# Performance work log

Measured on AMD Instinct MI355X. Metric: run time of the kernel, lower is better.

## Reference

```python
import jax, jax.numpy as jnp
import numpy as np

S, N, H = 4096, 32, 512

def setup_inputs() -> dict:
    key = jax.random.key(0)
    ks = jax.random.split(key, 8)
    scale = 1.0 / np.sqrt(H)
    return {
        "hidden": jax.random.normal(ks[0], (N, H), dtype=jnp.float32),
        "encoder_outputs": jax.random.normal(ks[1], (S, N, H), dtype=jnp.float32),
        "W_w": jax.random.uniform(ks[2], (H, H), jnp.float32, -scale, scale),
        "W_b": jax.random.uniform(ks[3], (H,), jnp.float32, -scale, scale),
        "U_w": jax.random.uniform(ks[4], (H, H), jnp.float32, -scale, scale),
        "U_b": jax.random.uniform(ks[5], (H,), jnp.float32, -scale, scale),
        "v_w": jax.random.uniform(ks[6], (1, H), jnp.float32, -scale, scale),
        "v_b": jax.random.uniform(ks[7], (1,), jnp.float32, -scale, scale),
    }

def reference(hidden, encoder_outputs, W_w, W_b, U_w, U_b, v_w, v_b):
    # W(hidden): [N,H] -> broadcast over seq dim (equivalent to expand then Linear)
    wh = hidden @ W_w.T + W_b                      # [N, H]
    ue = jnp.einsum('snh,kh->snk', encoder_outputs, U_w) + U_b  # [S, N, H]
    energy = jnp.tanh(wh[None, :, :] + ue)         # [S, N, H]
    score = jnp.einsum('snh,oh->sno', energy, v_w) + v_b        # [S, N, 1]
    attention_weights = jax.nn.softmax(score, axis=0)           # softmax over seq
    context = jnp.sum(attention_weights * encoder_outputs, axis=0)  # [N, H]
    return (context, attention_weights)
```

## Files before the change

kernel.cpp:

```cpp
#include <hip/hip_runtime.h>
#include <hip/hip_bf16.h>

#define Sdim 4096
#define Ndim 32
#define Hdim 512
#define Mdim (Sdim * Ndim)

#define BM 128
#define BN 256
#define BK 32

typedef __bf16 bf16x8 __attribute__((ext_vector_type(8)));
typedef float f32x4 __attribute__((ext_vector_type(4)));
typedef unsigned short ushort8v __attribute__((ext_vector_type(8)));

__device__ __forceinline__ void load_lds16(const void* g, void* l) {
    __builtin_amdgcn_global_load_lds(
        (const __attribute__((address_space(1))) void*)g,
        (__attribute__((address_space(3))) void*)l, 16, 0, 0);
}

__device__ __forceinline__ float ftanh(float x) {
    float e = __expf(2.f * x);
    return 1.f - 2.f / (e + 1.f);
}

__global__ __launch_bounds__(256) void k_prep_bias(
    const float* __restrict__ hidden, const float* __restrict__ Ww,
    const float* __restrict__ Wb, const float* __restrict__ Ubias,
    float* __restrict__ bias) {
    const int t = threadIdx.x, w = t >> 6, lane = t & 63;
    const int cc = blockIdx.x * 4 + w;
    const float4 w0 = *(const float4*)(Ww + (size_t)cc * Hdim + lane * 8);
    const float4 w1 = *(const float4*)(Ww + (size_t)cc * Hdim + lane * 8 + 4);
    const float wb = Wb[cc] + Ubias[cc];
    for (int n = 0; n < Ndim; ++n) {
        const float4 h0 = *(const float4*)(hidden + n * Hdim + lane * 8);
        const float4 h1 = *(const float4*)(hidden + n * Hdim + lane * 8 + 4);
        float p = w0.x * h0.x + w0.y * h0.y + w0.z * h0.z + w0.w * h0.w +
                  w1.x * h1.x + w1.y * h1.y + w1.z * h1.z + w1.w * h1.w;
        p += __shfl_xor(p, 1);  p += __shfl_xor(p, 2);
        p += __shfl_xor(p, 4);  p += __shfl_xor(p, 8);
        p += __shfl_xor(p, 16); p += __shfl_xor(p, 32);
        if (lane == 0) bias[n * Hdim + cc] = p + wb;
    }
}

__global__ __launch_bounds__(256) void k_cvt(
    const float* __restrict__ src, unsigned short* __restrict__ dst) {
    const int i = blockIdx.x * 256 + threadIdx.x;
    float4 v = ((const float4*)src)[i];
    union { __hip_bfloat162 h[2]; ushort4 u; } r;
    r.h[0] = __float22bfloat162_rn(make_float2(v.x, v.y));
    r.h[1] = __float22bfloat162_rn(make_float2(v.z, v.w));
    ((ushort4*)dst)[i] = r.u;
}

__global__ __launch_bounds__(512, 4) void k_gemm_score(
    const float* __restrict__ enc,
    const unsigned short* __restrict__ Ub,
    const float* __restrict__ bias,
    const float* __restrict__ vw,
    float* __restrict__ scorep) {
    __shared__ __align__(16) unsigned short Asm[BM][40];
    __shared__ __align__(16) unsigned short Bsm[BN * BK];
    __shared__ float ssm[4][BM];

    const int t = threadIdx.x;
    const int lane = t & 63;
    const int w = t >> 6;
    const int wM = w >> 2;
    const int wN = w & 3;
    const int c = lane & 15;
    const int q = lane >> 4;

    const int rowblk = blockIdx.x >> 1;
    const int colblk = blockIdx.x & 1;
    const int mBase = rowblk * BM;
    const int colBase = colblk * BN;

    const int ar = t >> 2;
    const int aq = t & 3;
    const int asw = ((ar >> 3) & 1) << 1;
    const float* aptr = enc + (size_t)(mBase + ar) * Hdim + aq * 8;
    unsigned short* awr = &Asm[ar][(aq ^ asw) * 8];

    const int bsw = (lane & 3) ^ ((lane >> 4) & 3);
    const unsigned short* bptr0 =
        Ub + (size_t)(colBase + w * 16 + (lane >> 2)) * Hdim + bsw * 8;
    const unsigned short* bptr1 =
        Ub + (size_t)(colBase + 128 + w * 16 + (lane >> 2)) * Hdim + bsw * 8;
    unsigned short* bdst0 = &Bsm[(w * 16) * BK];
    unsigned short* bdst1 = &Bsm[(128 + w * 16) * BK];

    const int sA = ((c >> 3) & 1) << 1;
    const int sB = c >> 2;

    f32x4 acc[4][4];
#pragma unroll
    for (int i = 0; i < 4; ++i)
#pragma unroll
        for (int j = 0; j < 4; ++j) acc[i][j] = (f32x4){0.f, 0.f, 0.f, 0.f};

    for (int kk = 0; kk < Hdim / BK; ++kk) {
        __syncthreads();
        const float4 f0 = *(const float4*)(aptr + kk * BK);
        const float4 f1 = *(const float4*)(aptr + kk * BK + 4);
        union { __hip_bfloat162 h[4]; ushort8v v; } pk;
        pk.h[0] = __float22bfloat162_rn(make_float2(f0.x, f0.y));
        pk.h[1] = __float22bfloat162_rn(make_float2(f0.z, f0.w));
        pk.h[2] = __float22bfloat162_rn(make_float2(f1.x, f1.y));
        pk.h[3] = __float22bfloat162_rn(make_float2(f1.z, f1.w));
        *(ushort8v*)awr = pk.v;
        load_lds16(bptr0 + kk * BK, bdst0);
        load_lds16(bptr1 + kk * BK, bdst1);
        __syncthreads();

        bf16x8 af[4], bfr[4];
#pragma unroll
        for (int mi = 0; mi < 4; ++mi)
            af[mi] = *(const bf16x8*)&Asm[wM * 64 + mi * 16 + c][(q ^ sA) * 8];
#pragma unroll
        for (int ni = 0; ni < 4; ++ni) {
            const int col = wN * 64 + ni * 16 + c;
            bfr[ni] = *(const bf16x8*)&Bsm[col * BK + (q ^ sB) * 8];
        }
#pragma unroll
        for (int mi = 0; mi < 4; ++mi)
#pragma unroll
            for (int ni = 0; ni < 4; ++ni)
                acc[mi][ni] = __builtin_amdgcn_mfma_f32_16x16x32_bf16(
                    af[mi], bfr[ni], acc[mi][ni], 0, 0, 0);
    }

    float vcol[4];
#pragma unroll
    for (int ni = 0; ni < 4; ++ni) vcol[ni] = vw[colBase + wN * 64 + ni * 16 + c];

#pragma unroll
    for (int mi = 0; mi < 4; ++mi) {
#pragma unroll
        for (int reg = 0; reg < 4; ++reg) {
            const int rl = wM * 64 + mi * 16 + q * 4 + reg;
            const int n = rl & 31;
            float p = 0.f;
#pragma unroll
            for (int ni = 0; ni < 4; ++ni) {
                const int col = colBase + wN * 64 + ni * 16 + c;
                float e = acc[mi][ni][reg] + bias[n * Hdim + col];
                p += vcol[ni] * ftanh(e);
            }
            p += __shfl_xor(p, 1);
            p += __shfl_xor(p, 2);
            p += __shfl_xor(p, 4);
            p += __shfl_xor(p, 8);
            if (c == 0) ssm[wN][rl] = p;
        }
    }
    __syncthreads();
    if (t < BM) {
        const int m = mBase + t;
        const float s = ssm[0][t] + ssm[1][t] + ssm[2][t] + ssm[3][t];
        scorep[colblk * Mdim + (m & 31) * Sdim + (m >> 5)] = s;
    }
}

__global__ __launch_bounds__(256) void k_softmax(
    const float* __restrict__ scorep,
    float* __restrict__ out_w) {
    const int n = blockIdx.x;
    const int t = threadIdx.x;
    const int w = t >> 6;
    __shared__ float row[Sdim];
    __shared__ float red[8];
    const float4* s0 = (const float4*)(scorep + n * Sdim);
    const float4* s1 = (const float4*)(scorep + Mdim + n * Sdim);

    float mx = -1e30f;
    for (int i = t; i < Sdim / 4; i += 256) {
        float4 a = s0[i], b = s1[i];
        float4 v;
        v.x = a.x + b.x; v.y = a.y + b.y; v.z = a.z + b.z; v.w = a.w + b.w;
        ((float4*)row)[i] = v;
        mx = fmaxf(mx, fmaxf(fmaxf(v.x, v.y), fmaxf(v.z, v.w)));
    }
#pragma unroll
    for (int o = 32; o > 0; o >>= 1) mx = fmaxf(mx, __shfl_xor(mx, o));
    if ((t & 63) == 0) red[w] = mx;
    __syncthreads();
    mx = fmaxf(fmaxf(red[0], red[1]), fmaxf(red[2], red[3]));

    float sum = 0.f;
    for (int i = t; i < Sdim; i += 256) sum += __expf(row[i] - mx);
#pragma unroll
    for (int o = 32; o > 0; o >>= 1) sum += __shfl_xor(sum, o);
    if ((t & 63) == 0) red[4 + w] = sum;
    __syncthreads();
    sum = red[4] + red[5] + red[6] + red[7];
    const float inv = 1.f / sum;
    for (int i = t; i < Sdim; i += 256)
        out_w[i * Ndim + n] = __expf(row[i] - mx) * inv;
}

__global__ __launch_bounds__(256) void k_context(
    const float* __restrict__ enc, const float* __restrict__ wts,
    float* __restrict__ part) {
    const int n = blockIdx.x & 31;
    const int sc = blockIdx.x >> 5;
    const int s0 = sc * 256;
    const int t = threadIdx.x;
    const int hv = t & 127;
    const int sl = t >> 7;
    float4 a0 = {0.f, 0.f, 0.f, 0.f}, a1 = {0.f, 0.f, 0.f, 0.f};
    for (int i = sl * 2; i < 256; i += 4) {
        const float w0 = wts[(size_t)(s0 + i) * Ndim + n];
        const float w1 = wts[(size_t)(s0 + i + 1) * Ndim + n];
        const float4 e0 =
            *(const float4*)(enc + ((size_t)(s0 + i) * Ndim + n) * Hdim + hv * 4);
        const float4 e1 =
            *(const float4*)(enc + ((size_t)(s0 + i + 1) * Ndim + n) * Hdim + hv * 4);
        a0.x += w0 * e0.x; a0.y += w0 * e0.y; a0.z += w0 * e0.z; a0.w += w0 * e0.w;
        a1.x += w1 * e1.x; a1.y += w1 * e1.y; a1.z += w1 * e1.z; a1.w += w1 * e1.w;
    }
    a0.x += a1.x; a0.y += a1.y; a0.z += a1.z; a0.w += a1.w;
    __shared__ float4 red[128];
    if (sl == 1) red[hv] = a0;
    __syncthreads();
    if (sl == 0) {
        const float4 b = red[hv];
        float4 r;
        r.x = a0.x + b.x; r.y = a0.y + b.y; r.z = a0.z + b.z; r.w = a0.w + b.w;
        *(float4*)(part + (size_t)(sc * 32 + n) * Hdim + hv * 4) = r;
    }
}

__global__ __launch_bounds__(256) void k_ctx_reduce(
    const float* __restrict__ part, float* __restrict__ out) {
    const int j = blockIdx.x * 256 + threadIdx.x;
    float4 s = {0.f, 0.f, 0.f, 0.f};
    for (int i = 0; i < 16; ++i) {
        const float4 v = ((const float4*)part)[i * 4096 + j];
        s.x += v.x; s.y += v.y; s.z += v.z; s.w += v.w;
    }
    ((float4*)out)[j] = s;
}

extern "C" void kernel_launch(void* const* d_in, const int* in_sizes, int n_in,
                              void* d_out, int out_size, void* d_ws,
                              size_t ws_size, hipStream_t stream) {
    const float* hidden = (const float*)d_in[0];
    const float* enc    = (const float*)d_in[1];
    const float* Ww     = (const float*)d_in[2];
    const float* Wb     = (const float*)d_in[3];
    const float* Uw     = (const float*)d_in[4];
    const float* Ubias  = (const float*)d_in[5];
    const float* vw     = (const float*)d_in[6];

    float* out = (float*)d_out;

    char* ws = (char*)d_ws;
    float* bias          = (float*)(ws);
    unsigned short* Ub16 = (unsigned short*)(ws + (64 << 10));
    float* scorep        = (float*)(ws + (576 << 10));
    float* part          = (float*)(ws + (64 << 10));

    k_prep_bias<<<128, 256, 0, stream>>>(hidden, Ww, Wb, Ubias, bias);
    k_cvt<<<256, 256, 0, stream>>>(Uw, Ub16);
    k_gemm_score<<<(Mdim / BM) * 2, 512, 0, stream>>>(enc, Ub16, bias, vw,
                                                      scorep);
    k_softmax<<<Ndim, 256, 0, stream>>>(scorep, out + Ndim * Hdim);
    k_context<<<Ndim * (Sdim / 256), 256, 0, stream>>>(enc, out + Ndim * Hdim,
                                                       part);
    k_ctx_reduce<<<16, 256, 0, stream>>>(part, out);
}
```

Before: 536.6 us.

## Double K-tile, prefetch A into registers, and widen context kernel blocks

The GEMM-score kernel's K tile grows from 32 to 64, halving the number of barrier-synchronised iterations. The next iteration's fp32 encoder slice is prefetched into registers while the current slice is converted to bf16 and written to LDS. Barriers are now raw s_barrier calls with explicit waitcnt and sched_barrier fences so the B-tile global-to-LDS loads overlap with the A conversion. The context kernel moves to 512 threads, with each lane handling 8 hidden elements over 8 sequence groups and a 7-way LDS reduction. The cost is more LDS per block (which may lower occupancy) and fragile hand-written waitcnt logic.

```diff
diff --git a/kernel.cpp b/kernel.cpp
--- a/kernel.cpp
+++ b/kernel.cpp
@@ -8,7 +8,7 @@
 
 #define BM 128
 #define BN 256
-#define BK 32
+#define BK 64
 
 typedef __bf16 bf16x8 __attribute__((ext_vector_type(8)));
 typedef float f32x4 __attribute__((ext_vector_type(4)));
@@ -62,7 +62,7 @@
     const float* __restrict__ bias,
     const float* __restrict__ vw,
     float* __restrict__ scorep) {
-    __shared__ __align__(16) unsigned short Asm[BM][40];
+    __shared__ __align__(16) unsigned short Asm[BM][72];
     __shared__ __align__(16) unsigned short Bsm[BN * BK];
     __shared__ float ssm[4][BM];
 
@@ -82,19 +82,18 @@
     const int ar = t >> 2;
     const int aq = t & 3;
     const int asw = ((ar >> 3) & 1) << 1;
-    const float* aptr = enc + (size_t)(mBase + ar) * Hdim + aq * 8;
-    unsigned short* awr = &Asm[ar][(aq ^ asw) * 8];
-
-    const int bsw = (lane & 3) ^ ((lane >> 4) & 3);
-    const unsigned short* bptr0 =
-        Ub + (size_t)(colBase + w * 16 + (lane >> 2)) * Hdim + bsw * 8;
-    const unsigned short* bptr1 =
-        Ub + (size_t)(colBase + 128 + w * 16 + (lane >> 2)) * Hdim + bsw * 8;
-    unsigned short* bdst0 = &Bsm[(w * 16) * BK];
-    unsigned short* bdst1 = &Bsm[(128 + w * 16) * BK];
+    const float4* arow =
+        (const float4*)(enc + (size_t)(mBase + ar) * Hdim) + aq * 4;
+    unsigned short* awr = &Asm[ar][((2 * aq) ^ asw) * 8];
+
+    const int coff = lane >> 3;
+    const int bch = (lane & 7) ^ coff;
+    const unsigned short* bsrc =
+        Ub + (size_t)(colBase + w * 8 + coff) * Hdim + bch * 8;
+    unsigned short* bdst = Bsm + (w * 8) * BK;
 
     const int sA = ((c >> 3) & 1) << 1;
-    const int sB = c >> 2;
+    const int sB = c & 7;
 
     f32x4 acc[4][4];
 #pragma unroll
@@ -102,40 +101,74 @@
 #pragma unroll
         for (int j = 0; j < 4; ++j) acc[i][j] = (f32x4){0.f, 0.f, 0.f, 0.f};
 
+    float4 a0 = arow[0], a1 = arow[1], a2 = arow[2], a3 = arow[3];
+
+#pragma unroll 1
     for (int kk = 0; kk < Hdim / BK; ++kk) {
-        __syncthreads();
-        const float4 f0 = *(const float4*)(aptr + kk * BK);
-        const float4 f1 = *(const float4*)(aptr + kk * BK + 4);
-        union { __hip_bfloat162 h[4]; ushort8v v; } pk;
-        pk.h[0] = __float22bfloat162_rn(make_float2(f0.x, f0.y));
-        pk.h[1] = __float22bfloat162_rn(make_float2(f0.z, f0.w));
-        pk.h[2] = __float22bfloat162_rn(make_float2(f1.x, f1.y));
-        pk.h[3] = __float22bfloat162_rn(make_float2(f1.z, f1.w));
-        *(ushort8v*)awr = pk.v;
-        load_lds16(bptr0 + kk * BK, bdst0);
-        load_lds16(bptr1 + kk * BK, bdst1);
-        __syncthreads();
-
-        bf16x8 af[4], bfr[4];
-#pragma unroll
-        for (int mi = 0; mi < 4; ++mi)
-            af[mi] = *(const bf16x8*)&Asm[wM * 64 + mi * 16 + c][(q ^ sA) * 8];
-#pragma unroll
-        for (int ni = 0; ni < 4; ++ni) {
-            const int col = wN * 64 + ni * 16 + c;
-            bfr[ni] = *(const bf16x8*)&Bsm[col * BK + (q ^ sB) * 8];
+        asm volatile("" ::: "memory");
+        __builtin_amdgcn_s_barrier();
+        asm volatile("" ::: "memory");
+        __builtin_amdgcn_sched_barrier(0);
+
+#pragma unroll
+        for (int g = 0; g < 4; ++g)
+            load_lds16(bsrc + (size_t)g * 64 * Hdim + kk * BK,
+                       bdst + g * 64 * BK);
+        asm volatile("" ::: "memory");
+        __builtin_amdgcn_sched_barrier(0);
+
+        union { __hip_bfloat162 h[4]; ushort8v v; } p0, p1;
+        p0.h[0] = __float22bfloat162_rn(make_float2(a0.x, a0.y));
+        p0.h[1] = __float22bfloat162_rn(make_float2(a0.z, a0.w));
+        p0.h[2] = __float22bfloat162_rn(make_float2(a1.x, a1.y));
+        p0.h[3] = __float22bfloat162_rn(make_float2(a1.z, a1.w));
+        p1.h[0] = __float22bfloat162_rn(make_float2(a2.x, a2.y));
+        p1.h[1] = __float22bfloat162_rn(make_float2(a2.z, a2.w));
+        p1.h[2] = __float22bfloat162_rn(make_float2(a3.x, a3.y));
+        p1.h[3] = __float22bfloat162_rn(make_float2(a3.z, a3.w));
+        *(ushort8v*)awr = p0.v;
+        *(ushort8v*)(awr + 8) = p1.v;
+
+        const int kn = (kk < Hdim / BK - 1) ? kk + 1 : kk;
+        const float4* ap = arow + kn * 16;
+        a0 = ap[0]; a1 = ap[1]; a2 = ap[2]; a3 = ap[3];
+
+        asm volatile("" ::: "memory");
+        __builtin_amdgcn_sched_barrier(0);
+        asm volatile("s_waitcnt vmcnt(4) lgkmcnt(0)" ::: "memory");
+        __builtin_amdgcn_s_barrier();
+        asm volatile("" ::: "memory");
+        __builtin_amdgcn_sched_barrier(0);
+
+#pragma unroll 1
+        for (int h = 0; h < 2; ++h) {
+            bf16x8 af[4], bfr[4];
+#pragma unroll
+            for (int mi = 0; mi < 4; ++mi) {
+                const int row = wM * 64 + mi * 16 + c;
+                af[mi] =
+                    *(const bf16x8*)&Asm[row][(((h << 2) | q) ^ sA) * 8];
+            }
+#pragma unroll
+            for (int ni = 0; ni < 4; ++ni) {
+                const int lc = wN * 64 + ni * 16 + c;
+                bfr[ni] = *(const bf16x8*)&Bsm[lc * BK +
+                                               (((h << 2) | q) ^ sB) * 8];
+            }
+#pragma unroll
+            for (int mi = 0; mi < 4; ++mi)
+#pragma unroll
+                for (int ni = 0; ni < 4; ++ni)
+                    acc[mi][ni] = __builtin_amdgcn_mfma_f32_16x16x32_bf16(
+                        af[mi], bfr[ni], acc[mi][ni], 0, 0, 0);
         }
-#pragma unroll
-        for (int mi = 0; mi < 4; ++mi)
-#pragma unroll
-            for (int ni = 0; ni < 4; ++ni)
-                acc[mi][ni] = __builtin_amdgcn_mfma_f32_16x16x32_bf16(
-                    af[mi], bfr[ni], acc[mi][ni], 0, 0, 0);
-    }
+    }
+    asm volatile("" :: "v"(a0.x), "v"(a1.x), "v"(a2.x), "v"(a3.x));
 
     float vcol[4];
 #pragma unroll
-    for (int ni = 0; ni < 4; ++ni) vcol[ni] = vw[colBase + wN * 64 + ni * 16 + c];
+    for (int ni = 0; ni < 4; ++ni)
+        vcol[ni] = vw[colBase + wN * 64 + ni * 16 + c];
 
 #pragma unroll
     for (int mi = 0; mi < 4; ++mi) {
@@ -202,35 +235,43 @@
         out_w[i * Ndim + n] = __expf(row[i] - mx) * inv;
 }
 
-__global__ __launch_bounds__(256) void k_context(
+__global__ __launch_bounds__(512) void k_context(
     const float* __restrict__ enc, const float* __restrict__ wts,
     float* __restrict__ part) {
     const int n = blockIdx.x & 31;
     const int sc = blockIdx.x >> 5;
     const int s0 = sc * 256;
     const int t = threadIdx.x;
-    const int hv = t & 127;
-    const int sl = t >> 7;
-    float4 a0 = {0.f, 0.f, 0.f, 0.f}, a1 = {0.f, 0.f, 0.f, 0.f};
-    for (int i = sl * 2; i < 256; i += 4) {
-        const float w0 = wts[(size_t)(s0 + i) * Ndim + n];
-        const float w1 = wts[(size_t)(s0 + i + 1) * Ndim + n];
-        const float4 e0 =
-            *(const float4*)(enc + ((size_t)(s0 + i) * Ndim + n) * Hdim + hv * 4);
-        const float4 e1 =
-            *(const float4*)(enc + ((size_t)(s0 + i + 1) * Ndim + n) * Hdim + hv * 4);
-        a0.x += w0 * e0.x; a0.y += w0 * e0.y; a0.z += w0 * e0.z; a0.w += w0 * e0.w;
-        a1.x += w1 * e1.x; a1.y += w1 * e1.y; a1.z += w1 * e1.z; a1.w += w1 * e1.w;
-    }
-    a0.x += a1.x; a0.y += a1.y; a0.z += a1.z; a0.w += a1.w;
-    __shared__ float4 red[128];
-    if (sl == 1) red[hv] = a0;
+    const int g = t >> 6;
+    const int lane = t & 63;
+    const int h0 = lane * 8;
+    float4 c0 = {0.f, 0.f, 0.f, 0.f}, c1 = {0.f, 0.f, 0.f, 0.f};
+#pragma unroll 4
+    for (int it = 0; it < 32; ++it) {
+        const int s = s0 + it * 8 + g;
+        const float wv = wts[(size_t)s * Ndim + n];
+        const float* e = enc + ((size_t)s * Ndim + n) * Hdim + h0;
+        const float4 e0 = *(const float4*)e;
+        const float4 e1 = *(const float4*)(e + 4);
+        c0.x += wv * e0.x; c0.y += wv * e0.y;
+        c0.z += wv * e0.z; c0.w += wv * e0.w;
+        c1.x += wv * e1.x; c1.y += wv * e1.y;
+        c1.z += wv * e1.z; c1.w += wv * e1.w;
+    }
+    __shared__ __align__(16) float4 red[7][128];
+    if (g > 0) { red[g - 1][lane * 2] = c0; red[g - 1][lane * 2 + 1] = c1; }
     __syncthreads();
-    if (sl == 0) {
-        const float4 b = red[hv];
-        float4 r;
-        r.x = a0.x + b.x; r.y = a0.y + b.y; r.z = a0.z + b.z; r.w = a0.w + b.w;
-        *(float4*)(part + (size_t)(sc * 32 + n) * Hdim + hv * 4) = r;
+    if (g == 0) {
+#pragma unroll
+        for (int i = 0; i < 7; ++i) {
+            const float4 b0 = red[i][lane * 2];
+            const float4 b1 = red[i][lane * 2 + 1];
+            c0.x += b0.x; c0.y += b0.y; c0.z += b0.z; c0.w += b0.w;
+            c1.x += b1.x; c1.y += b1.y; c1.z += b1.z; c1.w += b1.w;
+        }
+        float* o = part + (size_t)(sc * 32 + n) * Hdim + h0;
+        *(float4*)o = c0;
+        *(float4*)(o + 4) = c1;
     }
 }
 
@@ -269,7 +310,7 @@
     k_gemm_score<<<(Mdim / BM) * 2, 512, 0, stream>>>(enc, Ub16, bias, vw,
                                                       scorep);
     k_softmax<<<Ndim, 256, 0, stream>>>(scorep, out + Ndim * Hdim);
-    k_context<<<Ndim * (Sdim / 256), 256, 0, stream>>>(enc, out + Ndim * Hdim,
+    k_context<<<Ndim * (Sdim / 256), 512, 0, stream>>>(enc, out + Ndim * Hdim,
                                                        part);
     k_ctx_reduce<<<16, 256, 0, stream>>>(part, out);
 }
```

Result: faster. 483.1 us (-10.0%).
